# Kernel optimization log

Hardware: AMD Instinct MI355X
Metric: run time of the kernel (lower is better)

## Reference

```python
import jax, jax.numpy as jnp
import numpy as np

T, H = 2048, 2048            # tokens, hidden_size
NQ, NKV, D = 32, 4, 128      # q heads, kv heads, head_dim
E, K, I, CAP = 64, 8, 768, 512  # experts, top_k, moe_intermediate, per-expert capacity
EPS, THETA = 1e-6, 10000.0


def setup_inputs() -> dict:
    key = jax.random.key(0)
    ks = jax.random.split(key, 10)
    n = lambda k, shp, sc: jax.random.normal(k, shp, jnp.float32) * sc
    return {
        "hidden_states": n(ks[0], (T, H), 1.0),
        "positions": jnp.arange(T, dtype=jnp.int32),
        "wqkv": n(ks[1], (H, (NQ + 2 * NKV) * D), H ** -0.5),
        "wo": n(ks[2], (NQ * D, H), (NQ * D) ** -0.5),
        "q_norm_w": jnp.ones((D,), jnp.float32),
        "k_norm_w": jnp.ones((D,), jnp.float32),
        "ln1_w": jnp.ones((H,), jnp.float32),
        "ln2_w": jnp.ones((H,), jnp.float32),
        "gate_w": n(ks[3], (H, E), H ** -0.5),
        "w_gate": n(ks[4], (E, H, I), H ** -0.5),
        "w_up": n(ks[5], (E, H, I), H ** -0.5),
        "w_down": n(ks[6], (E, I, H), I ** -0.5),
    }


def _rmsnorm(x, w):
    v = jnp.mean(jnp.square(x.astype(jnp.float32)), axis=-1, keepdims=True)
    return (x.astype(jnp.float32) * jax.lax.rsqrt(v + EPS)).astype(x.dtype) * w


def _rope(x, cos, sin):
    # x: [T, heads, D]; neox-style rotate-half over full head_dim
    x1, x2 = x[..., : D // 2], x[..., D // 2:]
    c, s = cos[:, None, :], sin[:, None, :]
    return jnp.concatenate([x1 * c - x2 * s, x2 * c + x1 * s], axis=-1)


def _forward(hidden_states, positions, wqkv, wo, q_norm_w, k_norm_w, ln1_w, ln2_w, gate_w, w_gate, w_up, w_down):
    x = hidden_states
    # ---- input RMSNorm + GQA attention with QK-norm + RoPE ----
    h = _rmsnorm(x, ln1_w)
    qkv = h @ wqkv
    q, k, v = jnp.split(qkv, [NQ * D, NQ * D + NKV * D], axis=-1)
    q = _rmsnorm(q.reshape(T, NQ, D), q_norm_w)
    k = _rmsnorm(k.reshape(T, NKV, D), k_norm_w)
    v = v.reshape(T, NKV, D)
    inv_freq = 1.0 / (THETA ** (jnp.arange(0, D, 2, dtype=jnp.float32) / D))
    ang = positions.astype(jnp.float32)[:, None] * inv_freq  # [T, D/2]
    cos, sin = jnp.cos(ang), jnp.sin(ang)
    q, k = _rope(q, cos, sin), _rope(k, cos, sin)
    rep = NQ // NKV
    kr = jnp.repeat(k, rep, axis=1)  # [T, NQ, D]
    vr = jnp.repeat(v, rep, axis=1)
    scores = jnp.einsum('qhd,khd->hqk', q, kr) * (D ** -0.5)
    causal = jnp.tril(jnp.ones((T, T), bool))
    scores = jnp.where(causal[None], scores, -1e30)
    probs = jax.nn.softmax(scores, axis=-1)
    attn = jnp.einsum('hqk,khd->qhd', probs, vr).reshape(T, NQ * D)
    x = x + attn @ wo
    # ---- post-attn RMSNorm + sparse MoE (softmax top-k routing, renormalized) ----
    h = _rmsnorm(x, ln2_w)
    logits = h @ gate_w
    gate_probs = jax.nn.softmax(logits.astype(jnp.float32), axis=-1)
    topk_w, topk_idx = jax.lax.top_k(gate_probs, K)              # [T, K]
    topk_w = topk_w / jnp.sum(topk_w, axis=-1, keepdims=True)    # norm_topk_prob
    flat_e = topk_idx.reshape(-1)                                # [T*K], row-major
    oh = jax.nn.one_hot(flat_e, E, dtype=jnp.int32)
    pos = jnp.sum(jnp.cumsum(oh, axis=0) * oh, axis=-1) - 1      # slot within expert
    x_rep = jnp.repeat(h, K, axis=0)                             # [T*K, H]
    buf = jnp.zeros((E, CAP, H), h.dtype).at[flat_e, pos].set(x_rep, mode='drop')
    g = jnp.einsum('ech,ehi->eci', buf, w_gate)
    u = jnp.einsum('ech,ehi->eci', buf, w_up)
    act = jax.nn.silu(g) * u
    out_buf = jnp.einsum('eci,eih->ech', act, w_down)
    valid = (pos < CAP).astype(h.dtype)                          # CAP >> expected load; no drops in practice
    gathered = out_buf[flat_e, jnp.clip(pos, 0, CAP - 1)]        # [T*K, H]
    w = topk_w.reshape(-1).astype(h.dtype) * valid
    moe_out = jnp.sum((gathered * w[:, None]).reshape(T, K, H), axis=1)
    return x + moe_out


def reference(hidden_states, positions, wqkv, wo, q_norm_w, k_norm_w, ln1_w, ln2_w, gate_w, w_gate, w_up, w_down):
    return _forward(hidden_states, positions, wqkv, wo, q_norm_w, k_norm_w,
                    ln1_w, ln2_w, gate_w, w_gate, w_up, w_down)
```

## Files before the change

### kernel.cpp

```cpp
#include <hip/hip_runtime.h>
#include <hip/hip_bf16.h>

#define T_    2048
#define H_    2048
#define NQ_   32
#define NKV_  4
#define D_    128
#define E_    64
#define TK_   8
#define I_    768
#define CAP_  512
#define QKVW_ 5120

typedef float  f32x4  __attribute__((ext_vector_type(4)));
typedef __bf16 bf16x8 __attribute__((ext_vector_type(8)));
typedef int    i32x4  __attribute__((ext_vector_type(4)));
#define AS1 __attribute__((address_space(1)))
#define AS3 __attribute__((address_space(3)))

static __device__ __forceinline__ unsigned f2bf_u(float f){
  unsigned u = __builtin_bit_cast(unsigned, f);
  u += 0x7fffu + ((u >> 16) & 1u);
  return u >> 16;
}
static __device__ __forceinline__ float bf2f(unsigned h){
  unsigned u = h << 16;
  return __builtin_bit_cast(float, u);
}
struct HL { int h; int l; };
static __device__ __forceinline__ HL packsplit(float a, float b){
  unsigned ah = f2bf_u(a), bh = f2bf_u(b);
  float al = a - bf2f(ah), bl = b - bf2f(bh);
  HL r;
  r.h = (int)(ah | (bh << 16));
  r.l = (int)(f2bf_u(al) | (f2bf_u(bl) << 16));
  return r;
}
static __device__ __forceinline__ f32x4 mfma16(bf16x8 a, bf16x8 b, f32x4 c){
  return __builtin_amdgcn_mfma_f32_16x16x32_bf16(a, b, c, 0, 0, 0);
}

__global__ __launch_bounds__(256) void k_rms(const float* __restrict__ in,
                                             const float* __restrict__ w,
                                             unsigned short* __restrict__ outh,
                                             unsigned short* __restrict__ outl,
                                             float* __restrict__ cpy)
{
  const int t = blockIdx.x, tid = threadIdx.x;
  const float* row = in + (long)t * H_;
  float4 a = *(const float4*)(row + tid*8);
  float4 b = *(const float4*)(row + tid*8 + 4);
  float ss = a.x*a.x + a.y*a.y + a.z*a.z + a.w*a.w
           + b.x*b.x + b.y*b.y + b.z*b.z + b.w*b.w;
  #pragma unroll
  for (int o = 32; o >= 1; o >>= 1) ss += __shfl_xor(ss, o);
  __shared__ float red[4];
  if ((tid & 63) == 0) red[tid >> 6] = ss;
  __syncthreads();
  float tot = red[0] + red[1] + red[2] + red[3];
  float rs = rsqrtf(tot * (1.0f / (float)H_) + 1e-6f);
  const float* wp = w + tid*8;
  float vv[8] = {a.x, a.y, a.z, a.w, b.x, b.y, b.z, b.w};
  i32x4 oh, ol;
  #pragma unroll
  for (int d = 0; d < 4; d++){
    float v0 = vv[2*d]   * rs * wp[2*d];
    float v1 = vv[2*d+1] * rs * wp[2*d+1];
    HL r = packsplit(v0, v1);
    oh[d] = r.h; ol[d] = r.l;
  }
  *(i32x4*)(outh + (long)t * H_ + tid*8) = oh;
  if (outl) *(i32x4*)(outl + (long)t * H_ + tid*8) = ol;
  if (cpy){
    *(float4*)(cpy + (long)t * H_ + tid*8)     = a;
    *(float4*)(cpy + (long)t * H_ + tid*8 + 4) = b;
  }
}

__global__ __launch_bounds__(64) void k_ropetab(const int* __restrict__ pos,
                                                float* __restrict__ cosb,
                                                float* __restrict__ sinb)
{
  int t = blockIdx.x, j = threadIdx.x;
  float p = (float)pos[t];
  float freq = expf(-(float)j * (2.0f / (float)D_) * 9.210340371976184f);
  float ang = p * freq;
  cosb[t*64 + j] = cosf(ang);
  sinb[t*64 + j] = sinf(ang);
}

__global__ __launch_bounds__(256) void k_qknorm(const float* __restrict__ qkv,
                                                const float* __restrict__ qw,
                                                const float* __restrict__ kw,
                                                const float* __restrict__ cosb,
                                                const float* __restrict__ sinb,
                                                unsigned short* __restrict__ qh,
                                                unsigned short* __restrict__ ql,
                                                unsigned short* __restrict__ khp,
                                                unsigned short* __restrict__ klp)
{
  int gw = blockIdx.x*4 + (threadIdx.x >> 6);
  int lane = threadIdx.x & 63;
  int t = gw / 36, hh = gw - t*36;
  const float* src; const float* w;
  unsigned short *dh, *dl;
  if (hh < NQ_){
    src = qkv + (long)t*QKVW_ + hh*D_;
    w = qw;
    dh = qh + ((long)t*NQ_ + hh)*D_;
    dl = ql + ((long)t*NQ_ + hh)*D_;
  } else {
    int kh = hh - NQ_;
    src = qkv + (long)t*QKVW_ + NQ_*D_ + kh*D_;
    w = kw;
    dh = khp + ((long)t*NKV_ + kh)*D_;
    dl = klp + ((long)t*NKV_ + kh)*D_;
  }
  float a = src[lane], b = src[lane + 64];
  float ss = a*a + b*b;
  #pragma unroll
  for (int o = 32; o >= 1; o >>= 1) ss += __shfl_xor(ss, o);
  float rs = rsqrtf(ss * (1.0f / (float)D_) + 1e-6f);
  a *= rs * w[lane];
  b *= rs * w[lane + 64];
  float c = cosb[t*64 + lane], s = sinb[t*64 + lane];
  float r0 = a*c - b*s;
  float r1 = b*c + a*s;
  unsigned h0 = f2bf_u(r0), h1 = f2bf_u(r1);
  dh[lane]      = (unsigned short)h0;
  dh[lane + 64] = (unsigned short)h1;
  dl[lane]      = (unsigned short)f2bf_u(r0 - bf2f(h0));
  dl[lane + 64] = (unsigned short)f2bf_u(r1 - bf2f(h1));
}

__global__ __launch_bounds__(256) void k_vtrans(const float* __restrict__ qkv,
                                                unsigned short* __restrict__ vth,
                                                unsigned short* __restrict__ vtl)
{
  __shared__ unsigned short tileh[64][136];
  __shared__ unsigned short tilel[64][136];
  const int t0 = blockIdx.x * 64;
  const int hv = blockIdx.y;
  const int tid = threadIdx.x;
  #pragma unroll
  for (int it = 0; it < 8; it++){
    int chunk = tid + it*256;
    int r  = chunk >> 5;
    int c4 = chunk & 31;
    float4 v = *(const float4*)(qkv + (long)(t0 + r)*QKVW_ + (NQ_+NKV_)*D_ + hv*D_ + c4*4);
    float vals[4] = {v.x, v.y, v.z, v.w};
    #pragma unroll
    for (int q = 0; q < 4; q++){
      unsigned hi = f2bf_u(vals[q]);
      tileh[r][c4*4+q] = (unsigned short)hi;
      tilel[r][c4*4+q] = (unsigned short)f2bf_u(vals[q] - bf2f(hi));
    }
  }
  __syncthreads();
  int d = tid >> 1, hf = tid & 1;
  long dbase = ((long)(hv*D_ + d))*T_ + t0 + hf*32;
  #pragma unroll
  for (int k = 0; k < 4; k++){
    i32x4 oh, ol;
    #pragma unroll
    for (int d2 = 0; d2 < 4; d2++){
      int r0 = hf*32 + k*8 + d2*2, r1 = r0 + 1;
      oh[d2] = (int)((unsigned)tileh[r0][d] | ((unsigned)tileh[r1][d] << 16));
      ol[d2] = (int)((unsigned)tilel[r0][d] | ((unsigned)tilel[r1][d] << 16));
    }
    *(i32x4*)(vth + dbase + k*8) = oh;
    *(i32x4*)(vtl + dbase + k*8) = ol;
  }
}

__global__ __launch_bounds__(256,2) void k_attn(const unsigned short* __restrict__ qbh,
                                                const unsigned short* __restrict__ qbl,
                                                const unsigned short* __restrict__ kbh,
                                                const unsigned short* __restrict__ kbl,
                                                const unsigned short* __restrict__ vth,
                                                const unsigned short* __restrict__ vtl,
                                                unsigned short* __restrict__ abh,
                                                unsigned short* __restrict__ abl)
{
  __shared__ char ldsK[2][2][16384];
  const int b   = blockIdx.x;
  const int xcd = b & 7, kk = xcd >> 1;
  const int s_  = ((b >> 3) << 1) | (xcd & 1);
  const int h   = kk*8 + (s_ >> 4);
  const int p   = s_ & 15;
  const int hk  = kk;
  const int tid = threadIdx.x;
  const int wv  = tid >> 6, lane = tid & 63;
  const int l15 = lane & 15, g16 = lane >> 4;
  const float sc = 0.08838834764831845f;

  long gb[4];
  #pragma unroll
  for (int i = 0; i < 4; i++){
    int srow = i*16 + (tid >> 4);
    int c = (tid & 15) ^ (srow & 7);
    gb[i] = ((long)srow*NKV_ + hk)*D_ + c*8;
  }

  for (int ph = 0; ph < 2; ph++){
    const int qt  = ph ? p : (31 - p);
    const int q0  = qt*64 + wv*16;
    const int ntB = qt + 1;

    bf16x8 qfh[4], qfl[4];
    {
      long qoff = ((long)(q0 + l15)*NQ_ + h)*D_ + g16*8;
      #pragma unroll
      for (int ks = 0; ks < 4; ks++){
        qfh[ks] = *(const bf16x8*)(qbh + qoff + ks*32);
        qfl[ks] = *(const bf16x8*)(qbl + qoff + ks*32);
      }
    }

    f32x4 zz = {0.f,0.f,0.f,0.f};
    f32x4 o[8];
    #pragma unroll
    for (int dn = 0; dn < 8; dn++) o[dn] = zz;
    float m_run = -1e30f, l_run = 0.f;

    __syncthreads();
    #pragma unroll
    for (int i = 0; i < 4; i++){
      __builtin_amdgcn_global_load_lds((const AS1 int*)(kbh + gb[i]),
          (AS3 int*)((AS3 char*)&ldsK[0][0][0] + i*4096 + tid*16), 16, 0, 0);
      __builtin_amdgcn_global_load_lds((const AS1 int*)(kbl + gb[i]),
          (AS3 int*)((AS3 char*)&ldsK[0][1][0] + i*4096 + tid*16), 16, 0, 0);
    }

    for (int t = 0; t < ntB; t++){
      __syncthreads();
      const int kv0 = t*64;
      if (t+1 < ntB){
        long kadd = (long)(t+1)*64*NKV_*D_;
        int nb = (t+1) & 1;
        #pragma unroll
        for (int i = 0; i < 4; i++){
          __builtin_amdgcn_global_load_lds((const AS1 int*)(kbh + gb[i] + kadd),
              (AS3 int*)((AS3 char*)&ldsK[nb][0][0] + i*4096 + tid*16), 16, 0, 0);
          __builtin_amdgcn_global_load_lds((const AS1 int*)(kbl + gb[i] + kadd),
              (AS3 int*)((AS3 char*)&ldsK[nb][1][0] + i*4096 + tid*16), 16, 0, 0);
        }
      }
      {
        const char* Kh = &ldsK[t & 1][0][0];
        const char* Kl = &ldsK[t & 1][1][0];
        f32x4 sA[4];
        #pragma unroll
        for (int sub = 0; sub < 4; sub++) sA[sub] = zz;
        __builtin_amdgcn_s_setprio(1);
        #pragma unroll
        for (int sub = 0; sub < 4; sub++){
          int row = sub*16 + l15;
          int rsw = (row & 7) << 4;
          #pragma unroll
          for (int ks = 0; ks < 4; ks++){
            bf16x8 kh = *(const bf16x8*)(Kh + row*256 + (((ks*4 + g16)*16) ^ rsw));
            bf16x8 kl = *(const bf16x8*)(Kl + row*256 + (((ks*4 + g16)*16) ^ rsw));
            sA[sub] = mfma16(kh, qfl[ks], sA[sub]);
            sA[sub] = mfma16(kl, qfh[ks], sA[sub]);
            sA[sub] = mfma16(kh, qfh[ks], sA[sub]);
          }
        }
        __builtin_amdgcn_s_setprio(0);
        {
          int qrow = q0 + l15;
          float mt = -1e30f;
          #pragma unroll
          for (int sub = 0; sub < 4; sub++)
            #pragma unroll
            for (int r = 0; r < 4; r++){
              int kva = kv0 + sub*16 + g16*4 + r;
              float v = sA[sub][r]*sc;
              if (kva > qrow) v = -1e30f;
              sA[sub][r] = v;
              mt = fmaxf(mt, v);
            }
          mt = fmaxf(mt, __shfl_xor(mt,16));
          mt = fmaxf(mt, __shfl_xor(mt,32));
          float mnew = fmaxf(m_run, mt);
          float corr = __expf(m_run - mnew);
          float ps = 0.f;
          #pragma unroll
          for (int sub = 0; sub < 4; sub++)
            #pragma unroll
            for (int r = 0; r < 4; r++){
              float e = __expf(sA[sub][r] - mnew);
              sA[sub][r] = e;
              ps += e;
            }
          ps += __shfl_xor(ps,16);
          ps += __shfl_xor(ps,32);
          l_run = l_run*corr + ps;
          m_run = mnew;
          #pragma unroll
          for (int r = 0; r < 4; r++){
            float cr = __shfl(corr, g16*4 + r);
            #pragma unroll
            for (int dn = 0; dn < 8; dn++) o[dn][r] *= cr;
          }
        }
        #pragma unroll
        for (int kst = 0; kst < 2; kst++){
          bf16x8 pah, pal;
          {
            f32x4 s0 = sA[2*kst], s1 = sA[2*kst+1];
            i32x4 pkh, pkl;
            #pragma unroll
            for (int d = 0; d < 4; d++){
              const int e0 = 2*d, e1 = 2*d+1;
              int src0 = (((2*g16 + (e0>>2)) & 3) << 4) | l15;
              int src1 = (((2*g16 + (e1>>2)) & 3) << 4) | l15;
              float a0t = __shfl(s0[e0&3], src0), a1t = __shfl(s1[e0&3], src0);
              float b0t = __shfl(s0[e1&3], src1), b1t = __shfl(s1[e1&3], src1);
              float va = (g16 >= 2) ? a1t : a0t;
              float vb = (g16 >= 2) ? b1t : b0t;
              HL r = packsplit(va, vb);
              pkh[d] = r.h; pkl[d] = r.l;
            }
            pah = __builtin_bit_cast(bf16x8, pkh);
            pal = __builtin_bit_cast(bf16x8, pkl);
          }
          __builtin_amdgcn_s_setprio(1);
          #pragma unroll
          for (int dn = 0; dn < 8; dn++){
            long voff = ((long)(hk*D_ + dn*16 + l15))*T_ + kv0 + kst*32 + g16*8;
            bf16x8 bvh = *(const bf16x8*)(vth + voff);
            bf16x8 bvl = *(const bf16x8*)(vtl + voff);
            o[dn] = mfma16(pah, bvl, o[dn]);
            o[dn] = mfma16(pal, bvh, o[dn]);
            o[dn] = mfma16(pah, bvh, o[dn]);
          }
          __builtin_amdgcn_s_setprio(0);
        }
      }
    }

    {
      float linv = 1.0f / l_run;
      #pragma unroll
      for (int r = 0; r < 4; r++){
        float lr = __shfl(linv, g16*4 + r);
        long row = q0 + g16*4 + r;
        #pragma unroll
        for (int dn = 0; dn < 8; dn++){
          float v = o[dn][r]*lr;
          unsigned hi = f2bf_u(v);
          long idx = row*(NQ_*D_) + h*D_ + dn*16 + l15;
          abh[idx] = (unsigned short)hi;
          abl[idx] = (unsigned short)f2bf_u(v - bf2f(hi));
        }
      }
    }
  }
}

struct SA {
  const unsigned short* Ah;
  const unsigned short* Al;
  const float* B;
  int lda, ldb, K, ldc;
  float* Cf;
  const float* add;
};

template<int MODE>
__global__ __launch_bounds__(256,2) void k_gs(SA ga)
{
  __shared__ unsigned short ldsAh[128*64];
  __shared__ unsigned short ldsAl[128*64];
  __shared__ unsigned short ldsBh[8*128*8];
  __shared__ unsigned short ldsBl[8*128*8];
  const int tid = threadIdx.x;
  const int lane = tid & 63;
  const int wv = tid >> 6;
  const int wm = (wv >> 1)*64, wn = (wv & 1)*64;
  const int l15 = lane & 15, g16 = lane >> 4;

  const long m0 = (long)blockIdx.y * 128;
  const long n0 = (long)blockIdx.x * 128;

  long aoff[4];
  #pragma unroll
  for (int i = 0; i < 4; i++){
    int chunk = tid + i*256;
    int m = chunk >> 3, c = chunk & 7;
    aoff[i] = (m0 + m) * (long)ga.lda + c*8;
  }
  const float* brow = ga.B + n0 + (long)((tid >> 5)*8) * ga.ldb + (tid & 31)*4;

  f32x4 zz = {0.f,0.f,0.f,0.f};
  f32x4 acc[4][4];
  #pragma unroll
  for (int i = 0; i < 4; i++)
    #pragma unroll
    for (int j = 0; j < 4; j++) acc[i][j] = zz;

  i32x4 pva[4], pvl[4];
  float4 pb[8];
  #pragma unroll
  for (int i = 0; i < 4; i++){
    pva[i] = *(const i32x4*)(ga.Ah + aoff[i]);
    pvl[i] = *(const i32x4*)(ga.Al + aoff[i]);
  }
  #pragma unroll
  for (int r = 0; r < 8; r++) pb[r] = *(const float4*)(brow + (long)r * ga.ldb);

  for (int kt = 0; kt < ga.K; kt += 64){
    __syncthreads();
    #pragma unroll
    for (int i = 0; i < 4; i++){
      int chunk = tid + i*256;
      int m = chunk >> 3, c = chunk & 7;
      int sw = (c*16) ^ ((m & 7) << 4);
      *(i32x4*)((char*)ldsAh + m*128 + sw) = pva[i];
      *(i32x4*)((char*)ldsAl + m*128 + sw) = pvl[i];
    }
    {
      i32x4 ph0, ph1, ph2, ph3, pl0, pl1, pl2, pl3;
      #pragma unroll
      for (int r = 0; r < 8; r += 2){
        float4 va = pb[r];
        float4 vb = pb[r+1];
        int d = r >> 1;
        HL rx = packsplit(va.x, vb.x); ph0[d] = rx.h; pl0[d] = rx.l;
        HL ry = packsplit(va.y, vb.y); ph1[d] = ry.h; pl1[d] = ry.l;
        HL rz = packsplit(va.z, vb.z); ph2[d] = rz.h; pl2[d] = rz.l;
        HL rw = packsplit(va.w, vb.w); ph3[d] = rw.h; pl3[d] = rw.l;
      }
      int kbb = tid >> 5, nb = (tid & 31)*4;
      long bo = ((long)kbb*128 + nb) << 4;
      char* bph = (char*)ldsBh + bo;
      char* bpl = (char*)ldsBl + bo;
      *(i32x4*)(bph)      = ph0;  *(i32x4*)(bpl)      = pl0;
      *(i32x4*)(bph + 16) = ph1;  *(i32x4*)(bpl + 16) = pl1;
      *(i32x4*)(bph + 32) = ph2;  *(i32x4*)(bpl + 32) = pl2;
      *(i32x4*)(bph + 48) = ph3;  *(i32x4*)(bpl + 48) = pl3;
    }
    __syncthreads();
    if (kt + 64 < ga.K){
      #pragma unroll
      for (int i = 0; i < 4; i++){
        pva[i] = *(const i32x4*)(ga.Ah + aoff[i] + kt + 64);
        pvl[i] = *(const i32x4*)(ga.Al + aoff[i] + kt + 64);
      }
      #pragma unroll
      for (int r = 0; r < 8; r++) pb[r] = *(const float4*)(brow + (long)(kt + 64 + r) * ga.ldb);
    }
    #pragma unroll
    for (int ks = 0; ks < 2; ks++){
      bf16x8 afh[4], afl[4], bfh[4], bfl[4];
      #pragma unroll
      for (int i = 0; i < 4; i++){
        int m = wm + i*16 + l15;
        int sw = (ks*64 + g16*16) ^ ((m & 7) << 4);
        afh[i] = *(const bf16x8*)((const char*)ldsAh + m*128 + sw);
        afl[i] = *(const bf16x8*)((const char*)ldsAl + m*128 + sw);
      }
      #pragma unroll
      for (int j = 0; j < 4; j++){
        int n = wn + j*16 + l15;
        long bo = ((long)(ks*4 + g16)*128 + n) << 4;
        bfh[j] = *(const bf16x8*)((const char*)ldsBh + bo);
        bfl[j] = *(const bf16x8*)((const char*)ldsBl + bo);
      }
      #pragma unroll
      for (int i = 0; i < 4; i++)
        #pragma unroll
        for (int j = 0; j < 4; j++){
          acc[i][j] = mfma16(afh[i], bfl[j], acc[i][j]);
          acc[i][j] = mfma16(afl[i], bfh[j], acc[i][j]);
          acc[i][j] = mfma16(afh[i], bfh[j], acc[i][j]);
        }
    }
  }

  #pragma unroll
  for (int i = 0; i < 4; i++){
    #pragma unroll
    for (int j = 0; j < 4; j++){
      #pragma unroll
      for (int r = 0; r < 4; r++){
        float v = acc[i][j][r];
        long grow = m0 + wm + i*16 + g16*4 + r;
        long gcol = n0 + wn + j*16 + l15;
        long idx = grow * ga.ldc + gcol;
        if (MODE == 0) ga.Cf[idx] = v;
        else           ga.Cf[idx] = v + ga.add[idx];
      }
    }
  }
}

struct GA {
  const unsigned short* A;
  const float* B;
  const float* B2;
  int lda, ldb, K, ldc;
  unsigned short* Cb;
  const int* rowidx;
  const float* wslot;
  const int* counts;
  float* outp;
};

template<int MODE>
__global__ __launch_bounds__(256,3) void k_gemm(GA ga)
{
  __shared__ unsigned short ldsA[128*64];
  __shared__ unsigned short ldsB[8*128*8];
  const int tid = threadIdx.x;
  const int lane = tid & 63;
  const int wv = tid >> 6;
  const int l15 = lane & 15, g16 = lane >> 4;

  long m0 = (long)blockIdx.y * 128;
  long n0 = 0;
  const unsigned short* A = ga.A;
  const int* rowmap = nullptr;
  int nrows;
  int e = blockIdx.z, count = ga.counts[e];
  if ((int)m0 >= count) return;
  nrows = count;

  const float* bbase;
  {
    int c4 = (tid & 31) * 4;
    if (MODE == 2){
      n0 = (long)blockIdx.x * 64;
      rowmap = ga.rowidx + e * CAP_;
      if (c4 < 64) bbase = ga.B  + (long)e * H_ * I_ + n0 + c4;
      else         bbase = ga.B2 + (long)e * H_ * I_ + n0 + (c4 - 64);
    } else {
      n0 = (long)blockIdx.x * 128;
      bbase = ga.B + (long)e * I_ * H_ + n0 + c4;
      A = ga.A + (long)e * CAP_ * I_;
    }
  }

  const unsigned short* arow[4];
  #pragma unroll
  for (int i = 0; i < 4; i++){
    int chunk = tid + i*256;
    int m = chunk >> 3, c = chunk & 7;
    int csw = c ^ (m & 7);
    int s = (int)m0 + m; if (s > nrows - 1) s = nrows - 1;
    long row = (MODE == 2) ? (long)rowmap[s] : (long)s;
    arow[i] = A + row * (long)ga.lda + csw*8;
  }
  const float* brow = bbase + (long)((tid >> 5)*8) * ga.ldb;

  f32x4 zz = {0.f,0.f,0.f,0.f};
  f32x4 acc[2][8];
  #pragma unroll
  for (int i = 0; i < 2; i++)
    #pragma unroll
    for (int j = 0; j < 8; j++) acc[i][j] = zz;

  float4 pb[8];
  #pragma unroll
  for (int r = 0; r < 8; r++) pb[r] = *(const float4*)(brow + (long)r * ga.ldb);

  for (int kt = 0; kt < ga.K; kt += 64){
    __syncthreads();
    #pragma unroll
    for (int i = 0; i < 4; i++){
      __builtin_amdgcn_global_load_lds((const AS1 int*)(arow[i] + kt),
          (AS3 int*)((AS3 char*)ldsA + i*4096 + tid*16), 16, 0, 0);
    }
    {
      i32x4 p0, p1, p2, p3;
      #pragma unroll
      for (int r = 0; r < 8; r += 2){
        float4 va = pb[r];
        float4 vb = pb[r+1];
        int d = r >> 1;
        p0[d] = (int)(f2bf_u(va.x) | (f2bf_u(vb.x) << 16));
        p1[d] = (int)(f2bf_u(va.y) | (f2bf_u(vb.y) << 16));
        p2[d] = (int)(f2bf_u(va.z) | (f2bf_u(vb.z) << 16));
        p3[d] = (int)(f2bf_u(va.w) | (f2bf_u(vb.w) << 16));
      }
      int kbb = tid >> 5, nb = (tid & 31)*4;
      char* bp = (char*)ldsB + (((long)kbb*128 + nb) << 4);
      *(i32x4*)(bp)      = p0;
      *(i32x4*)(bp + 16) = p1;
      *(i32x4*)(bp + 32) = p2;
      *(i32x4*)(bp + 48) = p3;
    }
    __syncthreads();
    if (kt + 64 < ga.K){
      #pragma unroll
      for (int r = 0; r < 8; r++) pb[r] = *(const float4*)(brow + (long)(kt + 64 + r) * ga.ldb);
    }
    #pragma unroll
    for (int ks = 0; ks < 2; ks++){
      bf16x8 af[2], bfv[8];
      #pragma unroll
      for (int i = 0; i < 2; i++){
        int m = wv*32 + i*16 + l15;
        af[i] = *(const bf16x8*)((const char*)ldsA + m*128 + ((ks*64 + g16*16) ^ ((m & 7) << 4)));
      }
      #pragma unroll
      for (int j = 0; j < 8; j++){
        int n = j*16 + l15;
        bfv[j] = *(const bf16x8*)((const char*)ldsB + (((long)(ks*4 + g16)*128 + n) << 4));
      }
      #pragma unroll
      for (int i = 0; i < 2; i++)
        #pragma unroll
        for (int j = 0; j < 8; j++)
          acc[i][j] = mfma16(af[i], bfv[j], acc[i][j]);
    }
  }

  if (MODE == 2){
    #pragma unroll
    for (int i = 0; i < 2; i++){
      #pragma unroll
      for (int jj = 0; jj < 4; jj++){
        #pragma unroll
        for (int r = 0; r < 4; r++){
          float g = acc[i][jj][r];
          float u = acc[i][jj+4][r];
          float actv = g / (1.f + __expf(-g)) * u;
          int grow = (int)m0 + wv*32 + i*16 + g16*4 + r;
          if (grow < count)
            ga.Cb[((long)e*CAP_ + grow)*I_ + n0 + jj*16 + l15] = (unsigned short)f2bf_u(actv);
        }
      }
    }
  } else {
    #pragma unroll
    for (int i = 0; i < 2; i++){
      #pragma unroll
      for (int j = 0; j < 8; j++){
        #pragma unroll
        for (int r = 0; r < 4; r++){
          float v = acc[i][j][r];
          int grow = (int)m0 + wv*32 + i*16 + g16*4 + r;
          long gcol = n0 + j*16 + l15;
          if (grow < count){
            float ww = ga.wslot[e*CAP_ + grow];
            int tk = ga.rowidx[e*CAP_ + grow];
            atomicAdd(ga.outp + (long)tk*H_ + gcol, v*ww);
          }
        }
      }
    }
  }
}

__global__ __launch_bounds__(64) void k_router(const float* __restrict__ x2,
                                               const float* __restrict__ ln2w,
                                               const float* __restrict__ gwt,
                                               int* __restrict__ tidx,
                                               float* __restrict__ twv)
{
  __shared__ float hl[H_];
  __shared__ int   ti[8];
  __shared__ float tv[8];
  const int t = blockIdx.x, lane = threadIdx.x;
  const float* row = x2 + (long)t * H_;
  float ss = 0.f;
  #pragma unroll 4
  for (int j = 0; j < 32; j++){
    float v = row[j*64 + lane];
    hl[j*64 + lane] = v;
    ss += v*v;
  }
  #pragma unroll
  for (int o = 32; o >= 1; o >>= 1) ss += __shfl_xor(ss, o);
  float rs = rsqrtf(ss * (1.0f / (float)H_) + 1e-6f);
  __syncthreads();
  #pragma unroll 4
  for (int j = 0; j < 32; j++) hl[j*64 + lane] *= rs * ln2w[j*64 + lane];
  __syncthreads();
  float acc = 0.f;
  #pragma unroll 8
  for (int k = 0; k < H_; k++) acc += hl[k] * gwt[(long)k*E_ + lane];
  float mx = acc;
  #pragma unroll
  for (int o = 32; o >= 1; o >>= 1) mx = fmaxf(mx, __shfl_xor(mx, o));
  float p = __expf(acc - mx);
  float sm = p;
  #pragma unroll
  for (int o = 32; o >= 1; o >>= 1) sm += __shfl_xor(sm, o);
  p /= sm;
  float cur = p, wsum = 0.f;
  #pragma unroll
  for (int j = 0; j < 8; j++){
    float v = cur; int ix = lane;
    #pragma unroll
    for (int o = 1; o < 64; o <<= 1){
      float ov = __shfl_xor(v, o); int oi = __shfl_xor(ix, o);
      if (ov > v || (ov == v && oi < ix)){ v = ov; ix = oi; }
    }
    if (lane == ix) cur = -1.f;
    wsum += v;
    if (lane == 0){ ti[j] = ix; tv[j] = v; }
  }
  __syncthreads();
  if (lane < 8){
    tidx[t*TK_ + lane] = ti[lane];
    twv [t*TK_ + lane] = tv[lane] / wsum;
  }
}

__global__ __launch_bounds__(64) void k_route(const int* __restrict__ tidx,
                                              const float* __restrict__ twv,
                                              int* __restrict__ rowi,
                                              float* __restrict__ wsl,
                                              int* __restrict__ cnts)
{
  const int e = blockIdx.x, lane = threadIdx.x;
  int run = 0;
  for (int s0 = 0; s0 < T_*TK_; s0 += 64){
    int s = s0 + lane;
    int idx = tidx[s];
    bool m = (idx == e);
    unsigned long long mk = __ballot(m);
    int pre = __popcll(mk & ((1ull << lane) - 1ull));
    int pos = run + pre;
    if (m && pos < CAP_){
      rowi[e*CAP_ + pos] = s >> 3;
      wsl [e*CAP_ + pos] = twv[s];
    }
    run += __popcll(mk);
  }
  if (lane == 0) cnts[e] = (run < CAP_) ? run : CAP_;
}

extern "C" void kernel_launch(void* const* d_in, const int* in_sizes, int n_in,
                              void* d_out, int out_size, void* d_ws, size_t ws_size,
                              hipStream_t stream)
{
  (void)in_sizes; (void)n_in; (void)out_size; (void)ws_size;
  const float* x    = (const float*)d_in[0];
  const int*   pos  = (const int*)d_in[1];
  const float* wqkv = (const float*)d_in[2];
  const float* wo   = (const float*)d_in[3];
  const float* qnw  = (const float*)d_in[4];
  const float* knw  = (const float*)d_in[5];
  const float* ln1  = (const float*)d_in[6];
  const float* ln2  = (const float*)d_in[7];
  const float* gwt  = (const float*)d_in[8];
  const float* wg   = (const float*)d_in[9];
  const float* wu   = (const float*)d_in[10];
  const float* wd   = (const float*)d_in[11];
  float* out = (float*)d_out;

  char* ws = (char*)d_ws;
  size_t off = 0;
  auto alloc = [&](size_t b)->void*{ void* p = ws + off; off += (b + 255) & ~(size_t)255; return p; };

  unsigned short* hbh = (unsigned short*)alloc((size_t)T_*H_*2);
  unsigned short* hbl = (unsigned short*)alloc((size_t)T_*H_*2);
  float* qkv          = (float*)alloc((size_t)T_*QKVW_*4);
  float* cosb         = (float*)alloc((size_t)T_*64*4);
  float* sinb         = (float*)alloc((size_t)T_*64*4);
  unsigned short* qbh = (unsigned short*)alloc((size_t)T_*NQ_*D_*2);
  unsigned short* qbl = (unsigned short*)alloc((size_t)T_*NQ_*D_*2);
  unsigned short* kbh = (unsigned short*)alloc((size_t)T_*NKV_*D_*2);
  unsigned short* kbl = (unsigned short*)alloc((size_t)T_*NKV_*D_*2);
  unsigned short* vth = (unsigned short*)alloc((size_t)NKV_*D_*T_*2);
  unsigned short* vtl = (unsigned short*)alloc((size_t)NKV_*D_*T_*2);
  unsigned short* abh = (unsigned short*)alloc((size_t)T_*NQ_*D_*2);
  unsigned short* abl = (unsigned short*)alloc((size_t)T_*NQ_*D_*2);
  float* x2           = (float*)alloc((size_t)T_*H_*4);
  unsigned short* h2b = (unsigned short*)alloc((size_t)T_*H_*2);
  int* tidx           = (int*)alloc((size_t)T_*TK_*4);
  float* twv          = (float*)alloc((size_t)T_*TK_*4);
  int* rowi           = (int*)alloc((size_t)E_*CAP_*4);
  float* wsl          = (float*)alloc((size_t)E_*CAP_*4);
  int* cnts           = (int*)alloc((size_t)E_*4);
  unsigned short* gu  = (unsigned short*)alloc((size_t)E_*CAP_*I_*2);

  k_rms<<<T_, 256, 0, stream>>>(x, ln1, hbh, hbl, nullptr);
  k_ropetab<<<T_, 64, 0, stream>>>(pos, cosb, sinb);
  {
    SA a{}; a.Ah = hbh; a.Al = hbl; a.B = wqkv; a.lda = H_; a.ldb = QKVW_; a.K = H_; a.ldc = QKVW_; a.Cf = qkv;
    k_gs<0><<<dim3(QKVW_/128, T_/128), 256, 0, stream>>>(a);
  }
  k_qknorm<<<T_*36/4, 256, 0, stream>>>(qkv, qnw, knw, cosb, sinb, qbh, qbl, kbh, kbl);
  k_vtrans<<<dim3(T_/64, NKV_), 256, 0, stream>>>(qkv, vth, vtl);
  k_attn<<<512, 256, 0, stream>>>(qbh, qbl, kbh, kbl, vth, vtl, abh, abl);
  {
    SA a{}; a.Ah = abh; a.Al = abl; a.B = wo; a.lda = NQ_*D_; a.ldb = H_; a.K = NQ_*D_; a.ldc = H_;
    a.Cf = x2; a.add = x;
    k_gs<1><<<dim3(H_/128, T_/128), 256, 0, stream>>>(a);
  }
  k_rms<<<T_, 256, 0, stream>>>(x2, ln2, h2b, nullptr, out);
  k_router<<<T_, 64, 0, stream>>>(x2, ln2, gwt, tidx, twv);
  k_route<<<E_, 64, 0, stream>>>(tidx, twv, rowi, wsl, cnts);
  {
    GA a{}; a.A = h2b; a.B = wg; a.B2 = wu; a.lda = H_; a.ldb = I_; a.K = H_;
    a.Cb = gu; a.rowidx = rowi; a.counts = cnts;
    k_gemm<2><<<dim3(12, CAP_/128, E_), 256, 0, stream>>>(a);
  }
  {
    GA a{}; a.A = gu; a.B = wd; a.lda = I_; a.ldb = H_; a.K = I_;
    a.counts = cnts; a.rowidx = rowi; a.wslot = wsl; a.outp = out;
    k_gemm<3><<<dim3(H_/128, CAP_/128, E_), 256, 0, stream>>>(a);
  }
}
```

Measured before the change: 1.571 ms.

## Retile MoE expert GEMMs to 256-row by narrower-column blocks

Changes the MoE gate/up and down GEMM tiles from 128 rows by 64/128 columns to 256 rows by 32/64 columns, with each warp now covering 64 rows and 4x4 MFMA tiles. Since typical per-expert load fits in one 256-row block, each fp32 expert weight tile is fetched and converted to bf16 roughly once instead of per 128-row block. This trades more re-reads of the activation rows and narrower float2 weight loads for less weight traffic, and increases LDS use per block.

```diff
diff --git a/kernel.cpp b/kernel.cpp
--- a/kernel.cpp
+++ b/kernel.cpp
@@ -511,123 +511,115 @@
 template<int MODE>
 __global__ __launch_bounds__(256,3) void k_gemm(GA ga)
 {
-  __shared__ unsigned short ldsA[128*64];
-  __shared__ unsigned short ldsB[8*128*8];
+  __shared__ unsigned short ldsA[256*64];
+  __shared__ unsigned short ldsB[8*64*8];
   const int tid = threadIdx.x;
   const int lane = tid & 63;
   const int wv = tid >> 6;
   const int l15 = lane & 15, g16 = lane >> 4;
 
-  long m0 = (long)blockIdx.y * 128;
+  long m0 = (long)blockIdx.y * 256;
   long n0 = 0;
   const unsigned short* A = ga.A;
   const int* rowmap = nullptr;
-  int nrows;
   int e = blockIdx.z, count = ga.counts[e];
   if ((int)m0 >= count) return;
-  nrows = count;
 
   const float* bbase;
   {
-    int c4 = (tid & 31) * 4;
+    int c2 = (tid & 31) * 2;
     if (MODE == 2){
+      n0 = (long)blockIdx.x * 32;
+      rowmap = ga.rowidx + e * CAP_;
+      if (c2 < 32) bbase = ga.B  + (long)e * H_ * I_ + n0 + c2;
+      else         bbase = ga.B2 + (long)e * H_ * I_ + n0 + (c2 - 32);
+    } else {
       n0 = (long)blockIdx.x * 64;
-      rowmap = ga.rowidx + e * CAP_;
-      if (c4 < 64) bbase = ga.B  + (long)e * H_ * I_ + n0 + c4;
-      else         bbase = ga.B2 + (long)e * H_ * I_ + n0 + (c4 - 64);
-    } else {
-      n0 = (long)blockIdx.x * 128;
-      bbase = ga.B + (long)e * I_ * H_ + n0 + c4;
+      bbase = ga.B + (long)e * I_ * H_ + n0 + c2;
       A = ga.A + (long)e * CAP_ * I_;
     }
   }
 
-  const unsigned short* arow[4];
-  #pragma unroll
-  for (int i = 0; i < 4; i++){
+  const unsigned short* arow[8];
+  #pragma unroll
+  for (int i = 0; i < 8; i++){
     int chunk = tid + i*256;
     int m = chunk >> 3, c = chunk & 7;
     int csw = c ^ (m & 7);
-    int s = (int)m0 + m; if (s > nrows - 1) s = nrows - 1;
+    int s = (int)m0 + m; if (s > count - 1) s = count - 1;
     long row = (MODE == 2) ? (long)rowmap[s] : (long)s;
     arow[i] = A + row * (long)ga.lda + csw*8;
   }
   const float* brow = bbase + (long)((tid >> 5)*8) * ga.ldb;
 
   f32x4 zz = {0.f,0.f,0.f,0.f};
-  f32x4 acc[2][8];
-  #pragma unroll
-  for (int i = 0; i < 2; i++)
-    #pragma unroll
-    for (int j = 0; j < 8; j++) acc[i][j] = zz;
-
-  float4 pb[8];
-  #pragma unroll
-  for (int r = 0; r < 8; r++) pb[r] = *(const float4*)(brow + (long)r * ga.ldb);
+  f32x4 acc[4][4];
+  #pragma unroll
+  for (int i = 0; i < 4; i++)
+    #pragma unroll
+    for (int j = 0; j < 4; j++) acc[i][j] = zz;
+
+  float2 pb[8];
+  #pragma unroll
+  for (int r = 0; r < 8; r++) pb[r] = *(const float2*)(brow + (long)r * ga.ldb);
 
   for (int kt = 0; kt < ga.K; kt += 64){
     __syncthreads();
     #pragma unroll
-    for (int i = 0; i < 4; i++){
+    for (int i = 0; i < 8; i++){
       __builtin_amdgcn_global_load_lds((const AS1 int*)(arow[i] + kt),
           (AS3 int*)((AS3 char*)ldsA + i*4096 + tid*16), 16, 0, 0);
     }
     {
-      i32x4 p0, p1, p2, p3;
+      i32x4 p0, p1;
       #pragma unroll
       for (int r = 0; r < 8; r += 2){
-        float4 va = pb[r];
-        float4 vb = pb[r+1];
         int d = r >> 1;
-        p0[d] = (int)(f2bf_u(va.x) | (f2bf_u(vb.x) << 16));
-        p1[d] = (int)(f2bf_u(va.y) | (f2bf_u(vb.y) << 16));
-        p2[d] = (int)(f2bf_u(va.z) | (f2bf_u(vb.z) << 16));
-        p3[d] = (int)(f2bf_u(va.w) | (f2bf_u(vb.w) << 16));
-      }
-      int kbb = tid >> 5, nb = (tid & 31)*4;
-      char* bp = (char*)ldsB + (((long)kbb*128 + nb) << 4);
+        p0[d] = (int)(f2bf_u(pb[r].x) | (f2bf_u(pb[r+1].x) << 16));
+        p1[d] = (int)(f2bf_u(pb[r].y) | (f2bf_u(pb[r+1].y) << 16));
+      }
+      int kbb = tid >> 5, nb = (tid & 31)*2;
+      char* bp = (char*)ldsB + (((long)kbb*64 + nb) << 4);
       *(i32x4*)(bp)      = p0;
       *(i32x4*)(bp + 16) = p1;
-      *(i32x4*)(bp + 32) = p2;
-      *(i32x4*)(bp + 48) = p3;
     }
     __syncthreads();
     if (kt + 64 < ga.K){
       #pragma unroll
-      for (int r = 0; r < 8; r++) pb[r] = *(const float4*)(brow + (long)(kt + 64 + r) * ga.ldb);
+      for (int r = 0; r < 8; r++) pb[r] = *(const float2*)(brow + (long)(kt + 64 + r) * ga.ldb);
     }
     #pragma unroll
     for (int ks = 0; ks < 2; ks++){
-      bf16x8 af[2], bfv[8];
-      #pragma unroll
-      for (int i = 0; i < 2; i++){
-        int m = wv*32 + i*16 + l15;
+      bf16x8 af[4], bfv[4];
+      #pragma unroll
+      for (int i = 0; i < 4; i++){
+        int m = wv*64 + i*16 + l15;
         af[i] = *(const bf16x8*)((const char*)ldsA + m*128 + ((ks*64 + g16*16) ^ ((m & 7) << 4)));
       }
       #pragma unroll
-      for (int j = 0; j < 8; j++){
+      for (int j = 0; j < 4; j++){
         int n = j*16 + l15;
-        bfv[j] = *(const bf16x8*)((const char*)ldsB + (((long)(ks*4 + g16)*128 + n) << 4));
-      }
-      #pragma unroll
-      for (int i = 0; i < 2; i++)
+        bfv[j] = *(const bf16x8*)((const char*)ldsB + (((long)(ks*4 + g16)*64 + n) << 4));
+      }
+      #pragma unroll
+      for (int i = 0; i < 4; i++)
         #pragma unroll
-        for (int j = 0; j < 8; j++)
+        for (int j = 0; j < 4; j++)
           acc[i][j] = mfma16(af[i], bfv[j], acc[i][j]);
     }
   }
 
   if (MODE == 2){
     #pragma unroll
-    for (int i = 0; i < 2; i++){
-      #pragma unroll
-      for (int jj = 0; jj < 4; jj++){
+    for (int i = 0; i < 4; i++){
+      #pragma unroll
+      for (int jj = 0; jj < 2; jj++){
         #pragma unroll
         for (int r = 0; r < 4; r++){
           float g = acc[i][jj][r];
-          float u = acc[i][jj+4][r];
+          float u = acc[i][jj+2][r];
           float actv = g / (1.f + __expf(-g)) * u;
-          int grow = (int)m0 + wv*32 + i*16 + g16*4 + r;
+          int grow = (int)m0 + wv*64 + i*16 + g16*4 + r;
           if (grow < count)
             ga.Cb[((long)e*CAP_ + grow)*I_ + n0 + jj*16 + l15] = (unsigned short)f2bf_u(actv);
         }
@@ -635,13 +627,13 @@
     }
   } else {
     #pragma unroll
-    for (int i = 0; i < 2; i++){
-      #pragma unroll
-      for (int j = 0; j < 8; j++){
+    for (int i = 0; i < 4; i++){
+      #pragma unroll
+      for (int j = 0; j < 4; j++){
         #pragma unroll
         for (int r = 0; r < 4; r++){
           float v = acc[i][j][r];
-          int grow = (int)m0 + wv*32 + i*16 + g16*4 + r;
+          int grow = (int)m0 + wv*64 + i*16 + g16*4 + r;
           long gcol = n0 + j*16 + l15;
           if (grow < count){
             float ww = ga.wslot[e*CAP_ + grow];
@@ -799,11 +791,11 @@
   {
     GA a{}; a.A = h2b; a.B = wg; a.B2 = wu; a.lda = H_; a.ldb = I_; a.K = H_;
     a.Cb = gu; a.rowidx = rowi; a.counts = cnts;
-    k_gemm<2><<<dim3(12, CAP_/128, E_), 256, 0, stream>>>(a);
+    k_gemm<2><<<dim3(24, 2, E_), 256, 0, stream>>>(a);
   }
   {
     GA a{}; a.A = gu; a.B = wd; a.lda = I_; a.ldb = H_; a.K = I_;
     a.counts = cnts; a.rowidx = rowi; a.wslot = wsl; a.outp = out;
-    k_gemm<3><<<dim3(H_/128, CAP_/128, E_), 256, 0, stream>>>(a);
-  }
-}
+    k_gemm<3><<<dim3(32, 2, E_), 256, 0, stream>>>(a);
+  }
+}
```

Measured after the change: 1.489 ms. 1.06x faster.
